# Performance work log

Hardware: AMD Instinct MI355X
Metric: run time of the kernel (lower is better)

## Reference

```python
import jax, jax.numpy as jnp
import numpy as np

TEMPERATURE = 0.5
NEG_INF = -1e30  # mask value for diagonal in logsumexp (exact -inf also fine)


def _l2norm(x, eps=1e-12):
    # matches F.normalize(dim=1)
    n = jnp.sqrt(jnp.sum(x * x, axis=1, keepdims=True))
    return x / jnp.maximum(n, eps)


def setup_inputs() -> dict:
    key = jax.random.key(0)
    k1, k2, k3 = jax.random.split(key, 3)
    B, D, Q = 2048, 512, 32768
    return {
        "z_i": jax.random.normal(k1, (B, D), dtype=jnp.float32),
        "z_j": jax.random.normal(k2, (B, D), dtype=jnp.float32),
        "queue": jax.random.normal(k3, (Q, D), dtype=jnp.float32),
    }


def reference(z_i, z_j, queue):
    z = jnp.concatenate([z_i, z_j], axis=0)          # [N, D]
    N = z.shape[0]
    features = _l2norm(z)                            # [N, D]
    queue_norm = _l2norm(queue)                      # [Q, D]

    # NN retrieval from the support set
    sims_q = jnp.matmul(features, queue_norm.T)      # [N, Q]
    nn_idx = jnp.argmax(sims_q, axis=1)              # [N]
    nn_feats = queue_norm[nn_idx]                    # [N, D]

    # contrastive similarity between NNs and features
    sim = jnp.matmul(nn_feats, features.T) / TEMPERATURE  # [N, N]

    # positives: off-diagonals at +/- N//2
    sim_i_j = jnp.diagonal(sim, offset=N // 2)       # [N/2]
    sim_j_i = jnp.diagonal(sim, offset=-(N // 2))    # [N/2]
    positive_samples = jnp.concatenate([sim_i_j, sim_j_i], axis=0)  # [N]

    # negatives: all off-diagonal entries per row -> logsumexp with diag masked
    diag_mask = jnp.eye(N, dtype=bool)
    sim_masked = jnp.where(diag_mask, NEG_INF, sim)
    repulsion = jnp.mean(jax.scipy.special.logsumexp(sim_masked, axis=1))

    attraction = -jnp.mean(positive_samples)
    return attraction + repulsion
```

## Files before the change

### kernel.cpp

```cpp
#include <hip/hip_runtime.h>
#include <cstdint>

#define NFEAT 4096
#define NHALF 2048
#define DDIM  512
#define QROWS 32768

typedef unsigned short u16;
typedef unsigned char  u8;
typedef unsigned int   u32;
typedef unsigned long long u64;

typedef float  f32x16_t __attribute__((ext_vector_type(16)));
typedef int    i32x4_t  __attribute__((ext_vector_type(4)));
typedef int    i32x8_t  __attribute__((ext_vector_type(8)));

typedef const __attribute__((address_space(1))) void* gas_ptr;
typedef __attribute__((address_space(3))) void* las_ptr;

__device__ __forceinline__ u32 fkey(float f) {
  u32 u = __float_as_uint(f);
  return (u & 0x80000000u) ? ~u : (u | 0x80000000u);
}

__global__ void k_norm(const float* __restrict__ zi, const float* __restrict__ zj,
                       const float* __restrict__ queue,
                       u8* __restrict__ feat8T, u8* __restrict__ queue8T) {
  int gw = (int)((blockIdx.x * blockDim.x + threadIdx.x) >> 6);
  int lane = threadIdx.x & 63;
  const float* src; u8* dstT; int r31;
  if (gw < NFEAT) {
    src = (gw < NHALF) ? (zi + (size_t)gw * DDIM) : (zj + (size_t)(gw - NHALF) * DDIM);
    dstT = feat8T + (size_t)(gw >> 5) * 16384; r31 = gw & 31;
  } else {
    int r = gw - NFEAT;
    src = queue + (size_t)r * DDIM;
    dstT = queue8T + (size_t)(r >> 5) * 16384; r31 = r & 31;
  }
  float4 v0 = reinterpret_cast<const float4*>(src)[lane * 2];
  float4 v1 = reinterpret_cast<const float4*>(src)[lane * 2 + 1];
  float ss = v0.x*v0.x + v0.y*v0.y + v0.z*v0.z + v0.w*v0.w
           + v1.x*v1.x + v1.y*v1.y + v1.z*v1.z + v1.w*v1.w;
  #pragma unroll
  for (int off = 32; off >= 1; off >>= 1) ss += __shfl_xor(ss, off);
  float inv = 1.0f / fmaxf(sqrtf(ss), 1e-12f);
  float n0 = v0.x*inv, n1 = v0.y*inv, n2 = v0.z*inv, n3 = v0.w*inv;
  float n4 = v1.x*inv, n5 = v1.y*inv, n6 = v1.z*inv, n7 = v1.w*inv;
  u32 p01, p23, p45, p67;
  asm("v_cvt_pk_fp8_f32 %0, %1, %2" : "=v"(p01) : "v"(n0), "v"(n1));
  asm("v_cvt_pk_fp8_f32 %0, %1, %2" : "=v"(p23) : "v"(n2), "v"(n3));
  asm("v_cvt_pk_fp8_f32 %0, %1, %2" : "=v"(p45) : "v"(n4), "v"(n5));
  asm("v_cvt_pk_fp8_f32 %0, %1, %2" : "=v"(p67) : "v"(n6), "v"(n7));
  uint2 w8;
  w8.x = (p01 & 0xFFFFu) | (p23 << 16);
  w8.y = (p45 & 0xFFFFu) | (p67 << 16);
  size_t toff = (size_t)(lane >> 3) * 2048 + ((lane >> 2) & 1) * 1024
              + ((lane >> 1) & 1) * 512 + r31 * 16 + (lane & 1) * 8;
  *reinterpret_cast<uint2*>(dstT + toff) = w8;
}

#define SB0() __builtin_amdgcn_sched_barrier(0)
#define LGKM0_SB() do { asm volatile("s_waitcnt lgkmcnt(0)" ::: "memory"); SB0(); } while (0)
#define VMCNT4() asm volatile("s_waitcnt vmcnt(4)" ::: "memory")
#define VMCNT0() asm volatile("s_waitcnt vmcnt(0)" ::: "memory")
#define SBAR() __builtin_amdgcn_s_barrier()
#define RD(dst, base, off) asm volatile("ds_read_b128 %0, %1 offset:" off \
                                        : "=v"(dst) : "v"(base))

#define MFMA8(ACC, AV, BV) \
  ACC = __builtin_amdgcn_mfma_scale_f32_32x32x64_f8f6f4(AV, BV, ACC, 0, 0, 0, \
        0x7F7F7F7F, 0, 0x7F7F7F7F)

#define FP8_TILE(XA, XB) do { \
    i32x4_t a00, a01, a10, a11, b00, b01, b10, b11; \
    RD(a00, XA, "0"); RD(a01, XA, "512"); \
    RD(a10, XA, "2048"); RD(a11, XA, "2560"); \
    RD(b00, XB, "0"); RD(b01, XB, "512"); \
    RD(b10, XB, "2048"); RD(b11, XB, "2560"); \
    LGKM0_SB(); \
    i32x8_t A0 = __builtin_shufflevector(a00, a01, 0, 1, 2, 3, 4, 5, 6, 7); \
    i32x8_t A1 = __builtin_shufflevector(a10, a11, 0, 1, 2, 3, 4, 5, 6, 7); \
    i32x8_t B0 = __builtin_shufflevector(b00, b01, 0, 1, 2, 3, 4, 5, 6, 7); \
    i32x8_t B1 = __builtin_shufflevector(b10, b11, 0, 1, 2, 3, 4, 5, 6, 7); \
    __builtin_amdgcn_s_setprio(1); \
    MFMA8(acc00, A0, B0); \
    MFMA8(acc01, A0, B1); \
    MFMA8(acc10, A1, B0); \
    MFMA8(acc11, A1, B1); \
    __builtin_amdgcn_s_setprio(0); \
  } while (0)

#define FP8_MAIN_LOOP() do { \
  stage(0, 0); stage(1, 1); \
  VMCNT4(); \
  SBAR(); \
  _Pragma("unroll") \
  for (int t = 0; t < 8; t++) { \
    if (t <= 5) stage((t + 2) % 3, t + 2); \
    const u32 bb = (u32)((t % 3) * 16384); \
    FP8_TILE(aAd + bb, bAd + bb); \
    if (t < 7) { \
      if (t <= 5) VMCNT4(); else VMCNT0(); \
      SBAR(); \
    } \
  } } while (0)

__global__ __launch_bounds__(256, 2) void k_argmax_gemm8(
    const u8* __restrict__ feat8T, const u8* __restrict__ queue8T,
    u64* __restrict__ part) {
  __shared__ u8 lds[49152];
  const int tid = threadIdx.x;
  const int w = tid >> 6, lane = tid & 63;
  const int wr = w >> 1, wc = w & 1;
  const int l31 = lane & 31, hi = lane >> 5;
  const int bid = (int)blockIdx.x;
  const int wg = (bid & 7) * 1024 + (bid >> 3);
  const int mt = wg >> 5, ft = wg & 31;
  const int brow = mt * 128, bcol = ft * 128;

  const u8* pA = queue8T + (size_t)(brow >> 5) * 16384 + (tid >> 7) * 16384 + (tid & 127) * 16;
  const u8* pB = feat8T  + (size_t)(bcol >> 5) * 16384 + (tid >> 7) * 16384 + (tid & 127) * 16;
  const u32 dA = (u32)(size_t)(las_ptr)&lds[tid * 16];
  const u32 dB = dA + 8192;

  const u32 aAd = (u32)(size_t)(las_ptr)&lds[wr * 4096 + hi * 1024 + l31 * 16];
  const u32 bAd = (u32)(size_t)(las_ptr)&lds[8192 + wc * 4096 + hi * 1024 + l31 * 16];

  f32x16_t acc00 = {}, acc01 = {}, acc10 = {}, acc11 = {};

  auto stage = [&](int b, int t) {
    const u32 base = (u32)(b * 16384);
    __builtin_amdgcn_global_load_lds((gas_ptr)(pA + t * 2048),         (las_ptr)(size_t)(dA + base), 16, 0, 0);
    __builtin_amdgcn_global_load_lds((gas_ptr)(pA + 32768 + t * 2048), (las_ptr)(size_t)(dA + base + 4096), 16, 0, 0);
    __builtin_amdgcn_global_load_lds((gas_ptr)(pB + t * 2048),         (las_ptr)(size_t)(dB + base), 16, 0, 0);
    __builtin_amdgcn_global_load_lds((gas_ptr)(pB + 32768 + t * 2048), (las_ptr)(size_t)(dB + base + 4096), 16, 0, 0);
  };

  FP8_MAIN_LOOP();

  const int mslot = mt * 2 + wr;
  const int fbase = bcol + wc * 64 + l31;
  #pragma unroll
  for (int n = 0; n < 2; n++) {
    float bv = -3.0e38f; int br = 0;
    #pragma unroll
    for (int m = 0; m < 2; m++) {
      #pragma unroll
      for (int reg = 0; reg < 16; reg++) {
        float v = n == 0 ? (m == 0 ? acc00[reg] : acc10[reg])
                         : (m == 0 ? acc01[reg] : acc11[reg]);
        int lr = m * 32 + (reg & 3) + 8 * (reg >> 2);
        if (v > bv) { bv = v; br = lr; }
      }
    }
    u32 q = (u32)(brow + wr * 64 + br + 4 * hi);
    u64 key = ((u64)fkey(bv) << 32) | (u64)(0xFFFFFFFFu - q);
    u64 o = __shfl_xor(key, 32);
    key = key > o ? key : o;
    if (hi == 0) part[(size_t)(fbase + n * 32) * 512 + mslot] = key;
  }
}

__global__ void k_argmax_reduce(const u64* __restrict__ part, int* __restrict__ nnidx) {
  int row = (int)((blockIdx.x * blockDim.x + threadIdx.x) >> 6);
  int lane = threadIdx.x & 63;
  const u64* p = part + (size_t)row * 512;
  u64 best = 0;
  #pragma unroll
  for (int i = 0; i < 8; i++) { u64 v = p[lane * 8 + i]; best = best > v ? best : v; }
  #pragma unroll
  for (int off = 1; off < 64; off <<= 1) { u64 o = __shfl_xor(best, off); best = best > o ? best : o; }
  if (lane == 0) nnidx[row] = (int)(0xFFFFFFFFu - (u32)(best & 0xFFFFFFFFu));
}

__global__ void k_gather(const u8* __restrict__ queue8T, const int* __restrict__ nnidx,
                         u8* __restrict__ nn8T) {
  int T = (int)(blockIdx.x * blockDim.x + threadIdx.x);
  int rb = T >> 10;
  int c  = (T >> 5) & 31;
  int r  = T & 31;
  int g = nnidx[rb * 32 + r];
  const uint4 v = *reinterpret_cast<const uint4*>(
      queue8T + (size_t)(g >> 5) * 16384 + c * 512 + (g & 31) * 16);
  *reinterpret_cast<uint4*>(nn8T + (size_t)rb * 16384 + c * 512 + r * 16) = v;
}

__global__ __launch_bounds__(256, 2) void k_sim_gemm8(
    const u8* __restrict__ feat8T, const u8* __restrict__ nn8T,
    float2* __restrict__ lsep, float* __restrict__ pos) {
  __shared__ u8 lds[49152];
  const int tid = threadIdx.x;
  const int w = tid >> 6, lane = tid & 63;
  const int wr = w >> 1, wc = w & 1;
  const int l31 = lane & 31, hi = lane >> 5;
  const int bid = (int)blockIdx.x;
  const int wg = (bid & 7) * 128 + (bid >> 3);
  const int mt = wg >> 5, nt = wg & 31;
  const int mtb = mt * 128, ntb = nt * 128;

  const u8* pA = feat8T + (size_t)(mtb >> 5) * 16384 + (tid >> 7) * 16384 + (tid & 127) * 16;
  const u8* pB = nn8T   + (size_t)(ntb >> 5) * 16384 + (tid >> 7) * 16384 + (tid & 127) * 16;
  const u32 dA = (u32)(size_t)(las_ptr)&lds[tid * 16];
  const u32 dB = dA + 8192;

  const u32 aAd = (u32)(size_t)(las_ptr)&lds[wr * 4096 + hi * 1024 + l31 * 16];
  const u32 bAd = (u32)(size_t)(las_ptr)&lds[8192 + wc * 4096 + hi * 1024 + l31 * 16];

  f32x16_t acc00 = {}, acc01 = {}, acc10 = {}, acc11 = {};

  auto stage = [&](int b, int t) {
    const u32 base = (u32)(b * 16384);
    __builtin_amdgcn_global_load_lds((gas_ptr)(pA + t * 2048),         (las_ptr)(size_t)(dA + base), 16, 0, 0);
    __builtin_amdgcn_global_load_lds((gas_ptr)(pA + 32768 + t * 2048), (las_ptr)(size_t)(dA + base + 4096), 16, 0, 0);
    __builtin_amdgcn_global_load_lds((gas_ptr)(pB + t * 2048),         (las_ptr)(size_t)(dB + base), 16, 0, 0);
    __builtin_amdgcn_global_load_lds((gas_ptr)(pB + 32768 + t * 2048), (las_ptr)(size_t)(dB + base + 4096), 16, 0, 0);
  };

  FP8_MAIN_LOOP();

  const int mslot = mt * 2 + wr;
  const int ibase = mtb + wr * 64 + 4 * hi;
  #pragma unroll
  for (int n = 0; n < 2; n++) {
    const int j = ntb + wc * 64 + n * 32 + l31;
    const int jp = j ^ NHALF;
    float mx = -3.0e38f;
    #pragma unroll
    for (int m = 0; m < 2; m++) {
      #pragma unroll
      for (int reg = 0; reg < 16; reg++) {
        float v = (n == 0 ? (m == 0 ? acc00[reg] : acc10[reg])
                          : (m == 0 ? acc01[reg] : acc11[reg])) * 2.0f;
        int i = ibase + m * 32 + (reg & 3) + 8 * (reg >> 2);
        if (i == jp) pos[j] = v;
        if (i == j) v = -1.0e30f;
        mx = fmaxf(mx, v);
      }
    }
    float sm = 0.f;
    #pragma unroll
    for (int m = 0; m < 2; m++) {
      #pragma unroll
      for (int reg = 0; reg < 16; reg++) {
        float v = (n == 0 ? (m == 0 ? acc00[reg] : acc10[reg])
                          : (m == 0 ? acc01[reg] : acc11[reg])) * 2.0f;
        int i = ibase + m * 32 + (reg & 3) + 8 * (reg >> 2);
        if (i == j) v = -1.0e30f;
        sm += __expf(v - mx);
      }
    }
    float mo = __shfl_xor(mx, 32);
    float so = __shfl_xor(sm, 32);
    float M = fmaxf(mx, mo);
    sm = sm * __expf(mx - M) + so * __expf(mo - M);
    if (hi == 0) lsep[(size_t)j * 64 + mslot] = make_float2(M, sm);
  }
}

__global__ void k_lse(const float2* __restrict__ lsep, float* __restrict__ lse) {
  int row = (int)((blockIdx.x * blockDim.x + threadIdx.x) >> 6);
  int lane = threadIdx.x & 63;
  float2 p = lsep[(size_t)row * 64 + lane];
  float m = p.x, s = p.y;
  #pragma unroll
  for (int off = 1; off < 64; off <<= 1) {
    float mo = __shfl_xor(m, off), so = __shfl_xor(s, off);
    float M = fmaxf(m, mo);
    s = s * __expf(m - M) + so * __expf(mo - M);
    m = M;
  }
  if (lane == 0) lse[row] = m + __logf(s);
}

__global__ void k_final(const float* __restrict__ lse, const float* __restrict__ pos,
                        float* __restrict__ out) {
  __shared__ float red[4];
  int tid = threadIdx.x;
  float a = 0.f;
  for (int i = tid; i < NFEAT; i += 256) a += lse[i] - pos[i];
  #pragma unroll
  for (int off = 32; off >= 1; off >>= 1) a += __shfl_xor(a, off);
  if ((tid & 63) == 0) red[tid >> 6] = a;
  __syncthreads();
  if (tid == 0) out[0] = (red[0] + red[1] + red[2] + red[3]) / (float)NFEAT;
}

extern "C" void kernel_launch(void* const* d_in, const int* in_sizes, int n_in,
                              void* d_out, int out_size, void* d_ws, size_t ws_size,
                              hipStream_t stream) {
  const float* zi    = (const float*)d_in[0];
  const float* zj    = (const float*)d_in[1];
  const float* queue = (const float*)d_in[2];
  float* out = (float*)d_out;
  char* ws = (char*)d_ws;

  u8*     queue8T = (u8*)(ws + 0);
  u8*     feat8T  = (u8*)(ws + 16777216);
  u8*     nn8T    = (u8*)(ws + 18874368);
  u64*    part    = (u64*)(ws + 20971520);
  int*    nnidx   = (int*)(ws + 37748736);
  float2* lsep    = (float2*)(ws + 37765120);
  float*  pos     = (float*)(ws + 39862272);
  float*  lse     = (float*)(ws + 39878656);

  k_norm<<<9216, 256, 0, stream>>>(zi, zj, queue, feat8T, queue8T);
  k_argmax_gemm8<<<8192, 256, 0, stream>>>(feat8T, queue8T, part);
  k_argmax_reduce<<<1024, 256, 0, stream>>>(part, nnidx);
  k_gather<<<512, 256, 0, stream>>>(queue8T, nnidx, nn8T);
  k_sim_gemm8<<<1024, 256, 0, stream>>>(feat8T, nn8T, lsep, pos);
  k_lse<<<1024, 256, 0, stream>>>(lsep, lse);
  k_final<<<1, 256, 0, stream>>>(lse, pos, out);
}
```

Before: 114.0 us.

## Widen argmax GEMM tile to 128x256, double-buffer, and fuse reduce with gather

```diff
diff --git a/kernel.cpp b/kernel.cpp
--- a/kernel.cpp
+++ b/kernel.cpp
@@ -66,10 +66,120 @@
 #define SBAR() __builtin_amdgcn_s_barrier()
 #define RD(dst, base, off) asm volatile("ds_read_b128 %0, %1 offset:" off \
                                         : "=v"(dst) : "v"(base))
-
 #define MFMA8(ACC, AV, BV) \
   ACC = __builtin_amdgcn_mfma_scale_f32_32x32x64_f8f6f4(AV, BV, ACC, 0, 0, 0, \
         0x7F7F7F7F, 0, 0x7F7F7F7F)
+
+__global__ __launch_bounds__(256, 2) void k_argmax_gemm8(
+    const u8* __restrict__ feat8T, const u8* __restrict__ queue8T,
+    u64* __restrict__ part) {
+  __shared__ u8 lds[49152];
+  const int tid = threadIdx.x;
+  const int w = tid >> 6, lane = tid & 63;
+  const int wr = w >> 1, wc = w & 1;
+  const int l31 = lane & 31, hi = lane >> 5;
+  const int bid = (int)blockIdx.x;
+  const int wg = (bid & 7) * 512 + (bid >> 3);
+  const int mt = wg >> 4, ft = wg & 15;
+  const int brow = mt * 128, bcol = ft * 256;
+
+  const u8* pA = queue8T + (size_t)(brow >> 5) * 16384 + (tid >> 7) * 16384 + (tid & 127) * 16;
+  const u8* pB = feat8T  + (size_t)(bcol >> 5) * 16384 + (tid >> 7) * 16384 + (tid & 127) * 16;
+  const u32 dA = (u32)(size_t)(las_ptr)&lds[tid * 16];
+  const u32 dB = dA + 8192;
+
+  const u32 aAd = (u32)(size_t)(las_ptr)&lds[wr * 4096 + hi * 1024 + l31 * 16];
+  const u32 bAd = (u32)(size_t)(las_ptr)&lds[8192 + wc * 8192 + hi * 1024 + l31 * 16];
+
+  f32x16_t acc00 = {}, acc01 = {}, acc02 = {}, acc03 = {};
+  f32x16_t acc10 = {}, acc11 = {}, acc12 = {}, acc13 = {};
+
+  auto stage = [&](int b, int t) {
+    const u32 base = (u32)(b * 24576);
+    __builtin_amdgcn_global_load_lds((gas_ptr)(pA + t * 2048),         (las_ptr)(size_t)(dA + base), 16, 0, 0);
+    __builtin_amdgcn_global_load_lds((gas_ptr)(pA + 32768 + t * 2048), (las_ptr)(size_t)(dA + base + 4096), 16, 0, 0);
+    __builtin_amdgcn_global_load_lds((gas_ptr)(pB + t * 2048),         (las_ptr)(size_t)(dB + base), 16, 0, 0);
+    __builtin_amdgcn_global_load_lds((gas_ptr)(pB + 32768 + t * 2048), (las_ptr)(size_t)(dB + base + 4096), 16, 0, 0);
+    __builtin_amdgcn_global_load_lds((gas_ptr)(pB + 65536 + t * 2048), (las_ptr)(size_t)(dB + base + 8192), 16, 0, 0);
+    __builtin_amdgcn_global_load_lds((gas_ptr)(pB + 98304 + t * 2048), (las_ptr)(size_t)(dB + base + 12288), 16, 0, 0);
+  };
+
+  stage(0, 0);
+  VMCNT0();
+  SBAR();
+
+  #pragma unroll
+  for (int t = 0; t < 8; t++) {
+    if (t < 7) stage((t + 1) & 1, t + 1);
+    const u32 bb = (u32)((t & 1) * 24576);
+    const u32 xa = aAd + bb, xb = bAd + bb;
+    i32x4_t r0, r1, r2, r3, s0, s1, s2, s3, s4, s5, s6, s7;
+    RD(r0, xa, "0");    RD(r1, xa, "512");
+    RD(r2, xa, "2048"); RD(r3, xa, "2560");
+    RD(s0, xb, "0");    RD(s1, xb, "512");
+    RD(s2, xb, "2048"); RD(s3, xb, "2560");
+    RD(s4, xb, "4096"); RD(s5, xb, "4608");
+    RD(s6, xb, "6144"); RD(s7, xb, "6656");
+    LGKM0_SB();
+    i32x8_t A0 = __builtin_shufflevector(r0, r1, 0, 1, 2, 3, 4, 5, 6, 7);
+    i32x8_t A1 = __builtin_shufflevector(r2, r3, 0, 1, 2, 3, 4, 5, 6, 7);
+    i32x8_t B0 = __builtin_shufflevector(s0, s1, 0, 1, 2, 3, 4, 5, 6, 7);
+    i32x8_t B1 = __builtin_shufflevector(s2, s3, 0, 1, 2, 3, 4, 5, 6, 7);
+    i32x8_t B2 = __builtin_shufflevector(s4, s5, 0, 1, 2, 3, 4, 5, 6, 7);
+    i32x8_t B3 = __builtin_shufflevector(s6, s7, 0, 1, 2, 3, 4, 5, 6, 7);
+    __builtin_amdgcn_s_setprio(1);
+    MFMA8(acc00, A0, B0); MFMA8(acc01, A0, B1);
+    MFMA8(acc02, A0, B2); MFMA8(acc03, A0, B3);
+    MFMA8(acc10, A1, B0); MFMA8(acc11, A1, B1);
+    MFMA8(acc12, A1, B2); MFMA8(acc13, A1, B3);
+    __builtin_amdgcn_s_setprio(0);
+    if (t < 7) { VMCNT0(); SBAR(); }
+  }
+
+  const int mslot = mt * 2 + wr;
+#define AMAX_N(ACC0, ACC1, NOFF) do { \
+    float bv = -3.0e38f; int br = 0; \
+    _Pragma("unroll") \
+    for (int reg = 0; reg < 16; reg++) { \
+      float v = ACC0[reg]; int lr = (reg & 3) + 8 * (reg >> 2); \
+      if (v > bv) { bv = v; br = lr; } } \
+    _Pragma("unroll") \
+    for (int reg = 0; reg < 16; reg++) { \
+      float v = ACC1[reg]; int lr = 32 + (reg & 3) + 8 * (reg >> 2); \
+      if (v > bv) { bv = v; br = lr; } } \
+    u32 q = (u32)(brow + wr * 64 + br + 4 * hi); \
+    u64 key = ((u64)fkey(bv) << 32) | (u64)(0xFFFFFFFFu - q); \
+    u64 o = __shfl_xor(key, 32); \
+    key = key > o ? key : o; \
+    int j = bcol + wc * 128 + NOFF + l31; \
+    if (hi == 0) part[(size_t)j * 512 + mslot] = key; \
+  } while (0)
+  AMAX_N(acc00, acc10, 0);
+  AMAX_N(acc01, acc11, 32);
+  AMAX_N(acc02, acc12, 64);
+  AMAX_N(acc03, acc13, 96);
+#undef AMAX_N
+}
+
+__global__ void k_reduce_gather(const u64* __restrict__ part,
+                                const u8* __restrict__ queue8T,
+                                u8* __restrict__ nn8T) {
+  int row = (int)((blockIdx.x * blockDim.x + threadIdx.x) >> 6);
+  int lane = threadIdx.x & 63;
+  const u64* p = part + (size_t)row * 512;
+  u64 best = 0;
+  #pragma unroll
+  for (int i = 0; i < 8; i++) { u64 v = p[lane * 8 + i]; best = best > v ? best : v; }
+  #pragma unroll
+  for (int off = 1; off < 64; off <<= 1) { u64 o = __shfl_xor(best, off); best = best > o ? best : o; }
+  int g = (int)(0xFFFFFFFFu - (u32)(best & 0xFFFFFFFFu));
+  if (lane < 32) {
+    const uint4 v = *reinterpret_cast<const uint4*>(
+        queue8T + (size_t)(g >> 5) * 16384 + lane * 512 + (g & 31) * 16);
+    *reinterpret_cast<uint4*>(
+        nn8T + (size_t)(row >> 5) * 16384 + lane * 512 + (row & 31) * 16) = v;
+  }
+}
 
 #define FP8_TILE(XA, XB) do { \
     i32x4_t a00, a01, a10, a11, b00, b01, b10, b11; \
@@ -104,86 +214,6 @@
       SBAR(); \
     } \
   } } while (0)
-
-__global__ __launch_bounds__(256, 2) void k_argmax_gemm8(
-    const u8* __restrict__ feat8T, const u8* __restrict__ queue8T,
-    u64* __restrict__ part) {
-  __shared__ u8 lds[49152];
-  const int tid = threadIdx.x;
-  const int w = tid >> 6, lane = tid & 63;
-  const int wr = w >> 1, wc = w & 1;
-  const int l31 = lane & 31, hi = lane >> 5;
-  const int bid = (int)blockIdx.x;
-  const int wg = (bid & 7) * 1024 + (bid >> 3);
-  const int mt = wg >> 5, ft = wg & 31;
-  const int brow = mt * 128, bcol = ft * 128;
-
-  const u8* pA = queue8T + (size_t)(brow >> 5) * 16384 + (tid >> 7) * 16384 + (tid & 127) * 16;
-  const u8* pB = feat8T  + (size_t)(bcol >> 5) * 16384 + (tid >> 7) * 16384 + (tid & 127) * 16;
-  const u32 dA = (u32)(size_t)(las_ptr)&lds[tid * 16];
-  const u32 dB = dA + 8192;
-
-  const u32 aAd = (u32)(size_t)(las_ptr)&lds[wr * 4096 + hi * 1024 + l31 * 16];
-  const u32 bAd = (u32)(size_t)(las_ptr)&lds[8192 + wc * 4096 + hi * 1024 + l31 * 16];
-
-  f32x16_t acc00 = {}, acc01 = {}, acc10 = {}, acc11 = {};
-
-  auto stage = [&](int b, int t) {
-    const u32 base = (u32)(b * 16384);
-    __builtin_amdgcn_global_load_lds((gas_ptr)(pA + t * 2048),         (las_ptr)(size_t)(dA + base), 16, 0, 0);
-    __builtin_amdgcn_global_load_lds((gas_ptr)(pA + 32768 + t * 2048), (las_ptr)(size_t)(dA + base + 4096), 16, 0, 0);
-    __builtin_amdgcn_global_load_lds((gas_ptr)(pB + t * 2048),         (las_ptr)(size_t)(dB + base), 16, 0, 0);
-    __builtin_amdgcn_global_load_lds((gas_ptr)(pB + 32768 + t * 2048), (las_ptr)(size_t)(dB + base + 4096), 16, 0, 0);
-  };
-
-  FP8_MAIN_LOOP();
-
-  const int mslot = mt * 2 + wr;
-  const int fbase = bcol + wc * 64 + l31;
-  #pragma unroll
-  for (int n = 0; n < 2; n++) {
-    float bv = -3.0e38f; int br = 0;
-    #pragma unroll
-    for (int m = 0; m < 2; m++) {
-      #pragma unroll
-      for (int reg = 0; reg < 16; reg++) {
-        float v = n == 0 ? (m == 0 ? acc00[reg] : acc10[reg])
-                         : (m == 0 ? acc01[reg] : acc11[reg]);
-        int lr = m * 32 + (reg & 3) + 8 * (reg >> 2);
-        if (v > bv) { bv = v; br = lr; }
-      }
-    }
-    u32 q = (u32)(brow + wr * 64 + br + 4 * hi);
-    u64 key = ((u64)fkey(bv) << 32) | (u64)(0xFFFFFFFFu - q);
-    u64 o = __shfl_xor(key, 32);
-    key = key > o ? key : o;
-    if (hi == 0) part[(size_t)(fbase + n * 32) * 512 + mslot] = key;
-  }
-}
-
-__global__ void k_argmax_reduce(const u64* __restrict__ part, int* __restrict__ nnidx) {
-  int row = (int)((blockIdx.x * blockDim.x + threadIdx.x) >> 6);
-  int lane = threadIdx.x & 63;
-  const u64* p = part + (size_t)row * 512;
-  u64 best = 0;
-  #pragma unroll
-  for (int i = 0; i < 8; i++) { u64 v = p[lane * 8 + i]; best = best > v ? best : v; }
-  #pragma unroll
-  for (int off = 1; off < 64; off <<= 1) { u64 o = __shfl_xor(best, off); best = best > o ? best : o; }
-  if (lane == 0) nnidx[row] = (int)(0xFFFFFFFFu - (u32)(best & 0xFFFFFFFFu));
-}
-
-__global__ void k_gather(const u8* __restrict__ queue8T, const int* __restrict__ nnidx,
-                         u8* __restrict__ nn8T) {
-  int T = (int)(blockIdx.x * blockDim.x + threadIdx.x);
-  int rb = T >> 10;
-  int c  = (T >> 5) & 31;
-  int r  = T & 31;
-  int g = nnidx[rb * 32 + r];
-  const uint4 v = *reinterpret_cast<const uint4*>(
-      queue8T + (size_t)(g >> 5) * 16384 + c * 512 + (g & 31) * 16);
-  *reinterpret_cast<uint4*>(nn8T + (size_t)rb * 16384 + c * 512 + r * 16) = v;
-}
 
 __global__ __launch_bounds__(256, 2) void k_sim_gemm8(
     const u8* __restrict__ feat8T, const u8* __restrict__ nn8T,
@@ -298,15 +328,13 @@
   u8*     feat8T  = (u8*)(ws + 16777216);
   u8*     nn8T    = (u8*)(ws + 18874368);
   u64*    part    = (u64*)(ws + 20971520);
-  int*    nnidx   = (int*)(ws + 37748736);
-  float2* lsep    = (float2*)(ws + 37765120);
-  float*  pos     = (float*)(ws + 39862272);
-  float*  lse     = (float*)(ws + 39878656);
+  float2* lsep    = (float2*)(ws + 37748736);
+  float*  pos     = (float*)(ws + 39845888);
+  float*  lse     = (float*)(ws + 39862272);
 
   k_norm<<<9216, 256, 0, stream>>>(zi, zj, queue, feat8T, queue8T);
-  k_argmax_gemm8<<<8192, 256, 0, stream>>>(feat8T, queue8T, part);
-  k_argmax_reduce<<<1024, 256, 0, stream>>>(part, nnidx);
-  k_gather<<<512, 256, 0, stream>>>(queue8T, nnidx, nn8T);
+  k_argmax_gemm8<<<4096, 256, 0, stream>>>(feat8T, queue8T, part);
+  k_reduce_gather<<<1024, 256, 0, stream>>>(part, queue8T, nn8T);
   k_sim_gemm8<<<1024, 256, 0, stream>>>(feat8T, nn8T, lsep, pos);
   k_lse<<<1024, 256, 0, stream>>>(lsep, lse);
   k_final<<<1, 256, 0, stream>>>(lse, pos, out);
```

Result: faster. 109.5 us (-3.9%).
